# Optimization experiments

Measured on AMD Instinct MI355X. Metric: run time of the kernel, lower is better.

The kernel has to match this reference:

```python
import jax, jax.numpy as jnp
import numpy as np

N_LAYERS = 2
D_MODEL = 768
D_INNER = 1536
D_STATE = 16
D_CONV = 4
DT_RANK = 48
VOCAB = 50257
EPS = 1e-5


def _rms(x, w):
    return x * jax.lax.rsqrt(jnp.mean(x * x, axis=-1, keepdims=True) + EPS) * w


def _mixer(x, in_w, cw, cb, xp_w, dt_w, dt_b, a_log, d_skip, out_w):
    b, l, _ = x.shape
    xz = x @ in_w.T                                  # (b,l,2*d_in)
    u, z = jnp.split(xz, 2, axis=-1)                 # each (b,l,d_in)
    # causal depthwise conv1d
    uc = jax.lax.conv_general_dilated(
        u.transpose(0, 2, 1), cw[:, None, :], (1,), [(D_CONV - 1, 0)],
        feature_group_count=D_INNER, dimension_numbers=("NCH", "OIH", "NCH"))
    u = jax.nn.silu((uc + cb[:, None]).transpose(0, 2, 1))
    x_dbl = u @ xp_w.T                               # (b,l,dt_rank+2n)
    dt, B, C = jnp.split(x_dbl, [DT_RANK, DT_RANK + D_STATE], axis=-1)
    delta = jax.nn.softplus(dt @ dt_w.T + dt_b)      # (b,l,d_in)
    A = -jnp.exp(a_log)                              # (d_in,n)
    dA = jnp.exp(delta[..., None] * A)               # (b,l,d_in,n)
    dBu = delta[..., None] * B[:, :, None, :] * u[..., None]

    def step(h, inp):
        dA_t, dBu_t, C_t = inp
        h = dA_t * h + dBu_t
        return h, jnp.einsum("bdn,bn->bd", h, C_t)

    h0 = jnp.zeros((b, D_INNER, D_STATE), x.dtype)
    _, ys = jax.lax.scan(step, h0, (dA.transpose(1, 0, 2, 3),
                                    dBu.transpose(1, 0, 2, 3),
                                    C.transpose(1, 0, 2)))
    y = ys.transpose(1, 0, 2) + u * d_skip           # (b,l,d_in)
    y = y * jax.nn.silu(z)
    return y @ out_w.T


def setup_inputs() -> dict:
    key = jax.random.key(0)
    ks = jax.random.split(key, 12)
    std = 0.02
    emb = jax.random.normal(ks[0], (VOCAB, D_MODEL), jnp.float32) * std
    emb = emb.at[0].set(0.0)  # padding_idx=0
    tokens = jax.random.randint(ks[1], (2, 1024), 0, VOCAB)
    a_log = jnp.tile(jnp.log(jnp.arange(1, D_STATE + 1, dtype=jnp.float32)),
                     (N_LAYERS, D_INNER, 1))
    return {
        "tokens": tokens,
        "emb": emb,
        "norm_w": jnp.ones((N_LAYERS, D_MODEL), jnp.float32),
        "in_proj_w": jax.random.normal(ks[2], (N_LAYERS, 2 * D_INNER, D_MODEL), jnp.float32) * std,
        "conv_w": jax.random.normal(ks[3], (N_LAYERS, D_INNER, D_CONV), jnp.float32) * 0.1,
        "conv_b": jnp.zeros((N_LAYERS, D_INNER), jnp.float32),
        "x_proj_w": jax.random.normal(ks[4], (N_LAYERS, DT_RANK + 2 * D_STATE, D_INNER), jnp.float32) * std,
        "dt_proj_w": jax.random.normal(ks[5], (N_LAYERS, D_INNER, DT_RANK), jnp.float32) * (DT_RANK ** -0.5),
        "dt_proj_b": jax.random.uniform(ks[6], (N_LAYERS, D_INNER), jnp.float32, -4.6, -2.0),
        "A_log": a_log,
        "D": jnp.ones((N_LAYERS, D_INNER), jnp.float32),
        "out_proj_w": jax.random.normal(ks[7], (N_LAYERS, D_MODEL, D_INNER), jnp.float32) * (std / np.sqrt(2 * N_LAYERS)),
        "normf_w": jnp.ones((D_MODEL,), jnp.float32),
        "lm_head_w": jax.random.normal(ks[8], (VOCAB, D_MODEL), jnp.float32) * std,
    }


def reference(tokens, emb, norm_w, in_proj_w, conv_w, conv_b, x_proj_w,
              dt_proj_w, dt_proj_b, A_log, D, out_proj_w, normf_w, lm_head_w):
    x = emb[tokens]                                  # (b,l,d_model)
    for i in range(N_LAYERS):
        x = x + _mixer(_rms(x, norm_w[i]), in_proj_w[i], conv_w[i], conv_b[i],
                       x_proj_w[i], dt_proj_w[i], dt_proj_b[i], A_log[i],
                       D[i], out_proj_w[i])
    x = _rms(x, normf_w)
    return x @ lm_head_w.T                           # (b,l,vocab)
```

## Files before the change

### kernel.cpp

```cpp
#include <hip/hip_runtime.h>
#include <hip/hip_bf16.h>
#include <math.h>

#define DM 768
#define DI 1536
#define DSN 16
#define NB 2
#define SL 1024
#define MROWS 2048
#define VOC 50257
#define VOCP 50432
#define EPSR 1e-5f

typedef __attribute__((ext_vector_type(8))) short short8;
typedef __attribute__((ext_vector_type(4))) float f32x4;
typedef __attribute__((ext_vector_type(4))) unsigned short us4;
typedef unsigned short u16;

__device__ inline u16 f2bf(float f) {
    unsigned u = __builtin_bit_cast(unsigned, f);
    u += 0x7FFFu + ((u >> 16) & 1u);
    return (u16)(u >> 16);
}

#define G_LDS16(g, l) __builtin_amdgcn_global_load_lds( \
    (const __attribute__((address_space(1))) void*)(g), \
    (__attribute__((address_space(3))) void*)(l), 16, 0, 0)

__global__ __launch_bounds__(256)
void k_embed_rms(const int* __restrict__ tok, const float* __restrict__ emb,
                 const float* __restrict__ w, float* __restrict__ x,
                 u16* __restrict__ out) {
    int r = blockIdx.x;
    int t = tok[r];
    const float* src = emb + (size_t)t * DM;
    int c0 = threadIdx.x * 3;
    float v[3]; float ss = 0.f;
#pragma unroll
    for (int i = 0; i < 3; ++i) {
        v[i] = src[c0 + i]; ss += v[i] * v[i];
        x[(size_t)r * DM + c0 + i] = v[i];
    }
#pragma unroll
    for (int o = 32; o > 0; o >>= 1) ss += __shfl_down(ss, o);
    __shared__ float s[4];
    int lane = threadIdx.x & 63, wv = threadIdx.x >> 6;
    if (lane == 0) s[wv] = ss;
    __syncthreads();
    float sc = rsqrtf((s[0] + s[1] + s[2] + s[3]) / (float)DM + EPSR);
#pragma unroll
    for (int i = 0; i < 3; ++i)
        out[(size_t)r * DM + c0 + i] = f2bf(v[i] * sc * w[c0 + i]);
}

__global__ __launch_bounds__(256)
void k_rmsnorm_bf16(const float* __restrict__ x, const float* __restrict__ w,
                    u16* __restrict__ out) {
    int r = blockIdx.x;
    const float* row = x + (size_t)r * DM;
    int c0 = threadIdx.x * 3;
    float v[3]; float ss = 0.f;
#pragma unroll
    for (int i = 0; i < 3; ++i) { v[i] = row[c0 + i]; ss += v[i] * v[i]; }
#pragma unroll
    for (int o = 32; o > 0; o >>= 1) ss += __shfl_down(ss, o);
    __shared__ float s[4];
    int lane = threadIdx.x & 63, wv = threadIdx.x >> 6;
    if (lane == 0) s[wv] = ss;
    __syncthreads();
    float sc = rsqrtf((s[0] + s[1] + s[2] + s[3]) / (float)DM + EPSR);
#pragma unroll
    for (int i = 0; i < 3; ++i)
        out[(size_t)r * DM + c0 + i] = f2bf(v[i] * sc * w[c0 + i]);
}

struct CvtSeg { const float* src; u16* dst; int sr, sc, sld, dc, blk0, total4; };
struct CvtArgs { CvtSeg seg[9]; };

__global__ __launch_bounds__(256)
void k_cvt_multi(CvtArgs a) {
    int b = blockIdx.x;
    int s = 0;
#pragma unroll
    for (int q = 1; q < 9; ++q) if (a.seg[q].blk0 <= b) s = q;
    const CvtSeg& g = a.seg[s];
    long i4 = (long)(b - g.blk0) * 256 + threadIdx.x;
    if (i4 >= g.total4) return;
    long i = i4 * 4;
    int r = (int)(i / g.dc), c0 = (int)(i % g.dc);
    us4 o;
#pragma unroll
    for (int e = 0; e < 4; ++e) {
        int c = c0 + e;
        float v = (r < g.sr && c < g.sc) ? g.src[(size_t)r * g.sld + c] : 0.f;
        o[e] = f2bf(v);
    }
    *(us4*)&g.dst[i] = o;
}

__global__ void k_cvt_pad4(const float* __restrict__ src, u16* __restrict__ dst,
                           int sr, int sc, int sld, int dc, long total4) {
    long i4 = (long)blockIdx.x * 256 + threadIdx.x;
    if (i4 >= total4) return;
    long i = i4 * 4;
    int r = (int)(i / dc), c0 = (int)(i % dc);
    us4 o;
#pragma unroll
    for (int e = 0; e < 4; ++e) {
        int c = c0 + e;
        float v = (r < sr && c < sc) ? src[(size_t)r * sld + c] : 0.f;
        o[e] = f2bf(v);
    }
    *(us4*)&dst[i] = o;
}

__global__ void k_conv_silu(const float* __restrict__ xz, const float* __restrict__ cw,
                            const float* __restrict__ cb, float* __restrict__ uc,
                            u16* __restrict__ ucb) {
    int d = blockIdx.x * 256 + threadIdx.x;
    int r = blockIdx.y;
    int l = r & (SL - 1);
    float acc = cb[d];
#pragma unroll
    for (int j = 0; j < 4; ++j) {
        int ls = l - 3 + j;
        if (ls >= 0) acc += xz[(size_t)(r - 3 + j) * (2 * DI) + d] * cw[d * 4 + j];
    }
    float s = acc / (1.f + __expf(-acc));
    uc[(size_t)r * DI + d] = s;
    ucb[(size_t)r * DI + d] = f2bf(s);
}

__global__ __launch_bounds__(512)
void k_scan2(const float* __restrict__ delta, const float* __restrict__ uc,
             const float* __restrict__ xdbl, const float* __restrict__ xz,
             const float* __restrict__ alog, const float* __restrict__ Dp,
             u16* __restrict__ ybf) {
    __shared__ float ds2[8][16][20], us2[8][16][20], bn2[8][16][20], cn2[8][16][20];
    __shared__ float Sm[8][16][16], Pm[8][16][16];
    int b  = blockIdx.x / 96;
    int d0 = (blockIdx.x % 96) * 16;
    int tid = threadIdx.x, w = tid >> 6, lane = tid & 63;
    int ch = lane >> 2, nq = lane & 3;
    int d = d0 + ch;
    float A[4];
#pragma unroll
    for (int k = 0; k < 4; ++k) A[k] = -__expf(alog[d * DSN + nq + 4 * k]);
    int tb = w * 128;

    float h[4] = {0.f, 0.f, 0.f, 0.f};
    float sdl = 0.f;
    for (int t0 = 0; t0 < 128; t0 += 16) {
        int row0 = b * SL + tb + t0;
#pragma unroll
        for (int i = 0; i < 4; ++i) {
            int lin = i * 64 + lane, tt = lin >> 4, cc = lin & 15;
            size_t row = (size_t)(row0 + tt);
            ds2[w][cc][tt] = delta[row * DI + d0 + cc];
            us2[w][cc][tt] = uc[row * DI + d0 + cc];
            bn2[w][cc][tt] = xdbl[row * 128 + 48 + cc];
        }
#pragma unroll
        for (int g4 = 0; g4 < 4; ++g4) {
            f32x4 dl = *(const f32x4*)&ds2[w][ch][g4 * 4];
            f32x4 uv = *(const f32x4*)&us2[w][ch][g4 * 4];
            f32x4 bv[4];
#pragma unroll
            for (int k = 0; k < 4; ++k) bv[k] = *(const f32x4*)&bn2[w][nq + 4 * k][g4 * 4];
#pragma unroll
            for (int s = 0; s < 4; ++s) {
                float du = dl[s] * uv[s];
                sdl += dl[s];
#pragma unroll
                for (int k = 0; k < 4; ++k) {
                    float dA = __expf(dl[s] * A[k]);
                    h[k] = h[k] * dA + du * bv[k][s];
                }
            }
        }
    }
#pragma unroll
    for (int k = 0; k < 4; ++k) {
        Sm[w][ch][nq + 4 * k] = h[k];
        Pm[w][ch][nq + 4 * k] = __expf(A[k] * sdl);
    }
    __syncthreads();
    if (tid < 256) {
        int c2 = tid >> 4, n2 = tid & 15;
        float H = 0.f;
#pragma unroll
        for (int g = 0; g < 8; ++g) {
            float hi = H;
            H = Pm[g][c2][n2] * H + Sm[g][c2][n2];
            Sm[g][c2][n2] = hi;
        }
    }
    __syncthreads();
    float Dv = Dp[d];
#pragma unroll
    for (int k = 0; k < 4; ++k) h[k] = Sm[w][ch][nq + 4 * k];
    for (int t0 = 0; t0 < 128; t0 += 16) {
        int row0 = b * SL + tb + t0;
#pragma unroll
        for (int i = 0; i < 4; ++i) {
            int lin = i * 64 + lane, tt = lin >> 4, cc = lin & 15;
            size_t row = (size_t)(row0 + tt);
            ds2[w][cc][tt] = delta[row * DI + d0 + cc];
            us2[w][cc][tt] = uc[row * DI + d0 + cc];
            bn2[w][cc][tt] = xdbl[row * 128 + 48 + cc];
            cn2[w][cc][tt] = xdbl[row * 128 + 64 + cc];
        }
#pragma unroll
        for (int g4 = 0; g4 < 4; ++g4) {
            f32x4 dl = *(const f32x4*)&ds2[w][ch][g4 * 4];
            f32x4 uv = *(const f32x4*)&us2[w][ch][g4 * 4];
            f32x4 bv[4], cv[4];
#pragma unroll
            for (int k = 0; k < 4; ++k) {
                bv[k] = *(const f32x4*)&bn2[w][nq + 4 * k][g4 * 4];
                cv[k] = *(const f32x4*)&cn2[w][nq + 4 * k][g4 * 4];
            }
#pragma unroll
            for (int s = 0; s < 4; ++s) {
                float du = dl[s] * uv[s];
                float p = 0.f;
#pragma unroll
                for (int k = 0; k < 4; ++k) {
                    float dA = __expf(dl[s] * A[k]);
                    h[k] = h[k] * dA + du * bv[k][s];
                    p += h[k] * cv[k][s];
                }
                p += __shfl_xor(p, 1);
                p += __shfl_xor(p, 2);
                if (nq == 0) {
                    size_t row = (size_t)(row0 + g4 * 4 + s);
                    float z = xz[row * (2 * DI) + DI + d];
                    float y = p + uv[s] * Dv;
                    y *= z / (1.f + __expf(-z));
                    ybf[row * DI + d] = f2bf(y);
                }
            }
        }
    }
}

template <int EPIL>
__global__ __launch_bounds__(256)
void k_gemm_bt(const u16* __restrict__ A, const u16* __restrict__ W,
               float* C, const float* RES,
               const float* __restrict__ BIASV,
               int K, int ldc, int nTm) {
    __shared__ u16 Al[128 * 32];
    __shared__ u16 Wl[128 * 32];
    int nwg = gridDim.x;
    int qc = nwg >> 3, rc = nwg & 7;
    int xcd = blockIdx.x & 7, j = blockIdx.x >> 3;
    int wg = (xcd < rc ? xcd * (qc + 1) : rc * (qc + 1) + (xcd - rc) * qc) + j;
    int m0 = (wg % nTm) * 128, n0 = (wg / nTm) * 128;

    int tid = threadIdx.x, wave = tid >> 6, lane = tid & 63;
    int wm = wave >> 1, wn = wave & 1;
    f32x4 acc[4][4] = {};
    const int rS = (lane >> 2);
    const int kS = (((lane & 3) ^ ((lane >> 3) & 3)) * 8);
    const int kofs = (((lane >> 4) ^ ((lane >> 1) & 3)) * 8);
    const int fr = lane & 15;

    for (int k0 = 0; k0 < K; k0 += 32) {
#pragma unroll
        for (int i = 0; i < 2; ++i) {
            int rowA = m0 + wave * 32 + i * 16 + rS;
            G_LDS16(A + (size_t)rowA * K + k0 + kS, &Al[wave * 1024 + i * 512]);
            int rowW = n0 + wave * 32 + i * 16 + rS;
            G_LDS16(W + (size_t)rowW * K + k0 + kS, &Wl[wave * 1024 + i * 512]);
        }
        __syncthreads();
        short8 af[4], bfr[4];
#pragma unroll
        for (int f = 0; f < 4; ++f) {
            af[f]  = *(const short8*)&Al[(wm * 64 + f * 16 + fr) * 32 + kofs];
            bfr[f] = *(const short8*)&Wl[(wn * 64 + f * 16 + fr) * 32 + kofs];
        }
#pragma unroll
        for (int i = 0; i < 4; ++i)
#pragma unroll
            for (int jj = 0; jj < 4; ++jj)
                acc[i][jj] = __builtin_amdgcn_mfma_f32_16x16x32_bf16(af[i], bfr[jj], acc[i][jj], 0, 0, 0);
        __syncthreads();
    }
    int r4 = (lane >> 4) * 4;
#pragma unroll
    for (int i = 0; i < 4; ++i)
#pragma unroll
        for (int jj = 0; jj < 4; ++jj) {
            int col = n0 + wn * 64 + jj * 16 + fr;
            float bia = (EPIL == 2) ? BIASV[col] : 0.f;
#pragma unroll
            for (int rr = 0; rr < 4; ++rr) {
                int row = m0 + wm * 64 + i * 16 + r4 + rr;
                size_t off = (size_t)row * ldc + col;
                float v = acc[i][jj][rr];
                if (EPIL == 1) v += RES[off];
                if (EPIL == 2) { v += bia; v = (v > 20.f) ? v : log1pf(__expf(v)); }
                C[off] = v;
            }
        }
}

#define BAR  __builtin_amdgcn_s_barrier()
#define LGK0 do { asm volatile("s_waitcnt lgkmcnt(0)" ::: "memory"); \
                  __builtin_amdgcn_sched_barrier(0); } while (0)
#define VMC6 asm volatile("s_waitcnt vmcnt(6)" ::: "memory")
#define VMC0 asm volatile("s_waitcnt vmcnt(0)" ::: "memory")

#define STAGE_HT(t, op, half, GB, RB) do {                                   \
    const u16* _g = (GB) + (size_t)((RB) + (half) * 128 + (w << 3) + srow) * K \
                    + (t) * 64 + scol;                                        \
    G_LDS16(_g, &lds[(t) & 1][op][half][w << 9]);                             \
    G_LDS16(_g + (size_t)64 * K, &lds[(t) & 1][op][half][4096 + (w << 9)]);   \
} while (0)

#define RD_A(dst, t, mq) do {                                                \
    _Pragma("unroll") for (int _m = 0; _m < 4; ++_m)                          \
    _Pragma("unroll") for (int _k = 0; _k < 2; ++_k)                          \
        dst[_m][_k] = *(const short8*)&lds[(t) & 1][0][wm]                    \
            [(mq) * 4096 + _m * 1024 + (rd_off ^ (_k << 5))];                 \
} while (0)

#define RD_B(t, nq) do {                                                     \
    _Pragma("unroll") for (int _n = 0; _n < 2; ++_n)                          \
    _Pragma("unroll") for (int _k = 0; _k < 2; ++_k)                          \
        bfv[_n][_k] = *(const short8*)&lds[(t) & 1][1][wbh]                   \
            [wbr * 4096 + (nq) * 2048 + _n * 1024 + (rd_off ^ (_k << 5))];    \
} while (0)

#define MM16(AF, mq, nq) do {                                                \
    __builtin_amdgcn_s_setprio(1);                                           \
    _Pragma("unroll") for (int _m = 0; _m < 4; ++_m)                          \
    _Pragma("unroll") for (int _n = 0; _n < 2; ++_n)                          \
    _Pragma("unroll") for (int _k = 0; _k < 2; ++_k)                          \
        acc[(mq) * 4 + _m][(nq) * 2 + _n] =                                   \
            __builtin_amdgcn_mfma_f32_16x16x32_bf16(                          \
                AF[_m][_k], bfv[_n][_k], acc[(mq) * 4 + _m][(nq) * 2 + _n],   \
                0, 0, 0);                                                     \
    __builtin_amdgcn_s_setprio(0);                                           \
} while (0)

template <int K>
__global__ __launch_bounds__(512, 2)
void k_gemm256(const u16* __restrict__ Ap, const u16* __restrict__ Wp,
               float* __restrict__ C, int ldc, int nmax, int nTm) {
    constexpr int NT = K / 64;
    constexpr int NI = NT / 2;
    __shared__ __align__(16) u16 lds[2][2][2][8192];

    int per8 = gridDim.x >> 3;
    int wg = (blockIdx.x & 7) * per8 + (blockIdx.x >> 3);
    int m0 = (wg % nTm) * 256, n0 = (wg / nTm) * 256;

    int tid = threadIdx.x, w = tid >> 6, lane = tid & 63;
    int wm = w >> 2, wn = w & 3, wbh = wn >> 1, wbr = wn & 1;
    int fr = lane & 15;
    int sw = (fr & 1) * 32 + ((fr >> 1) & 1) * 16 + ((fr >> 2) & 1) * 8;
    int rd_off = fr * 64 + (((lane >> 4) * 8) ^ sw);
    int srow = lane >> 3;
    int scol = ((lane & 7) * 8) ^ (((lane >> 3) & 1) * 32 + ((lane >> 4) & 1) * 16 +
                                   ((lane >> 5) & 1) * 8);

    f32x4 acc[8][4] = {};
    short8 af0[4][2], af1[4][2], bfv[2][2];

    STAGE_HT(0, 0, 0, Ap, m0); STAGE_HT(0, 0, 1, Ap, m0);
    STAGE_HT(0, 1, 0, Wp, n0); STAGE_HT(0, 1, 1, Wp, n0);
    STAGE_HT(1, 0, 0, Ap, m0); STAGE_HT(1, 0, 1, Ap, m0);
    STAGE_HT(1, 1, 0, Wp, n0);
    VMC6; BAR;

    for (int i = 0; i < NI - 1; ++i) {
        const int ta = 2 * i, tb = 2 * i + 1;
        RD_A(af0, ta, 0); RD_B(ta, 0);
        STAGE_HT(tb, 1, 1, Wp, n0);
        BAR; LGK0; MM16(af0, 0, 0); BAR;
        RD_A(af1, ta, 1);
        STAGE_HT(ta + 2, 0, 0, Ap, m0);
        BAR; LGK0; MM16(af1, 1, 0); BAR;
        RD_B(ta, 1);
        STAGE_HT(ta + 2, 0, 1, Ap, m0);
        BAR; LGK0; MM16(af1, 1, 1); BAR;
        STAGE_HT(ta + 2, 1, 0, Wp, n0);
        BAR; MM16(af0, 0, 1); VMC6; BAR;
        RD_A(af0, tb, 0); RD_B(tb, 0);
        STAGE_HT(ta + 2, 1, 1, Wp, n0);
        BAR; LGK0; MM16(af0, 0, 0); BAR;
        RD_A(af1, tb, 1);
        STAGE_HT(ta + 3, 0, 0, Ap, m0);
        BAR; LGK0; MM16(af1, 1, 0); BAR;
        RD_B(tb, 1);
        STAGE_HT(ta + 3, 0, 1, Ap, m0);
        BAR; LGK0; MM16(af1, 1, 1); BAR;
        STAGE_HT(ta + 3, 1, 0, Wp, n0);
        BAR; MM16(af0, 0, 1); VMC6; BAR;
    }
    {
        const int ta = NT - 2, tb = NT - 1;
        RD_A(af0, ta, 0); RD_B(ta, 0);
        STAGE_HT(tb, 1, 1, Wp, n0);
        BAR; LGK0; MM16(af0, 0, 0); BAR;
        RD_A(af1, ta, 1);
        BAR; LGK0; MM16(af1, 1, 0); BAR;
        RD_B(ta, 1);
        BAR; LGK0; MM16(af1, 1, 1); BAR;
        BAR; MM16(af0, 0, 1); VMC0; BAR;
        RD_A(af0, tb, 0); RD_B(tb, 0);
        BAR; LGK0; MM16(af0, 0, 0); BAR;
        RD_A(af1, tb, 1);
        BAR; LGK0; MM16(af1, 1, 0); BAR;
        RD_B(tb, 1);
        BAR; LGK0; MM16(af1, 1, 1); BAR;
        BAR; MM16(af0, 0, 1); BAR;
    }

    int r4 = (lane >> 4) * 4;
#pragma unroll
    for (int mi = 0; mi < 8; ++mi)
#pragma unroll
        for (int ni = 0; ni < 4; ++ni) {
            int col = n0 + wn * 64 + (ni >> 1) * 32 + (ni & 1) * 16 + fr;
            if (col >= nmax) continue;
            int row = m0 + wm * 128 + (mi >> 2) * 64 + (mi & 3) * 16 + r4;
#pragma unroll
            for (int rr = 0; rr < 4; ++rr)
                C[(size_t)(row + rr) * ldc + col] = acc[mi][ni][rr];
        }
}

extern "C" void kernel_launch(void* const* d_in, const int* in_sizes, int n_in,
                              void* d_out, int out_size, void* d_ws, size_t ws_size,
                              hipStream_t stream) {
    (void)in_sizes; (void)n_in; (void)out_size;
    const int*   tok   = (const int*)d_in[0];
    const float* emb   = (const float*)d_in[1];
    const float* normw = (const float*)d_in[2];
    const float* inw   = (const float*)d_in[3];
    const float* cw    = (const float*)d_in[4];
    const float* cb    = (const float*)d_in[5];
    const float* xpw   = (const float*)d_in[6];
    const float* dtw   = (const float*)d_in[7];
    const float* dtb   = (const float*)d_in[8];
    const float* alog  = (const float*)d_in[9];
    const float* Dp    = (const float*)d_in[10];
    const float* outw  = (const float*)d_in[11];
    const float* normf = (const float*)d_in[12];
    const float* lmw   = (const float*)d_in[13];
    float* out = (float*)d_out;

    char* p = (char*)d_ws;
    auto alloc = [&](size_t bytes) { char* r = p; p += (bytes + 255) & ~(size_t)255; return r; };
    float* x     = (float*)alloc((size_t)MROWS * DM * 4);
    u16*   xnb   = (u16*)  alloc((size_t)MROWS * DM * 2);
    float* xz    = (float*)alloc((size_t)MROWS * 2 * DI * 4);
    float* uc    = (float*)alloc((size_t)MROWS * DI * 4);
    u16*   ucb   = (u16*)  alloc((size_t)MROWS * DI * 2);
    float* xdbl  = (float*)alloc((size_t)MROWS * 128 * 4);
    u16*   xdblb = (u16*)  alloc((size_t)MROWS * 64 * 2);
    float* delta = (float*)alloc((size_t)MROWS * DI * 4);
    u16*   ybf   = (u16*)  alloc((size_t)MROWS * DI * 2);
    u16*   winb  = (u16*)  alloc((size_t)NB * (2 * DI) * DM * 2);
    u16*   wxpb  = (u16*)  alloc((size_t)NB * 128 * DI * 2);
    u16*   wdtb  = (u16*)  alloc((size_t)NB * DI * 64 * 2);
    u16*   woutb = (u16*)  alloc((size_t)NB * DM * DI * 2);
    u16*   wlmb  = (u16*)  alloc((size_t)VOCP * DM * 2);
    if ((size_t)(p - (char*)d_ws) > ws_size) return;

    CvtArgs ca;
    int blk = 0;
    auto seg = [&](int idx, const float* s, u16* d, int sr, int sc, int sld, int dc, int dr) {
        int t4 = dr * dc / 4;
        ca.seg[idx] = CvtSeg{s, d, sr, sc, sld, dc, blk, t4};
        blk += (t4 + 255) / 256;
    };
    seg(0, lmw, wlmb, VOC, DM, DM, DM, VOCP);
    seg(1, inw,                          winb,                          2 * DI, DM, DM, DM, 2 * DI);
    seg(2, inw + (size_t)2 * DI * DM,    winb + (size_t)2 * DI * DM,    2 * DI, DM, DM, DM, 2 * DI);
    seg(3, xpw,                          wxpb,                          80, DI, DI, DI, 128);
    seg(4, xpw + (size_t)80 * DI,        wxpb + (size_t)128 * DI,       80, DI, DI, DI, 128);
    seg(5, dtw,                          wdtb,                          DI, 48, 48, 64, DI);
    seg(6, dtw + (size_t)DI * 48,        wdtb + (size_t)DI * 64,        DI, 48, 48, 64, DI);
    seg(7, outw,                         woutb,                         DM, DI, DI, DI, DM);
    seg(8, outw + (size_t)DM * DI,       woutb + (size_t)DM * DI,       DM, DI, DI, DI, DM);
    k_cvt_multi<<<dim3(blk), 256, 0, stream>>>(ca);

    k_embed_rms<<<MROWS, 256, 0, stream>>>(tok, emb, normw, x, xnb);

    for (int i = 0; i < NB; ++i) {
        if (i > 0)
            k_rmsnorm_bf16<<<MROWS, 256, 0, stream>>>(x, normw + i * DM, xnb);

        k_gemm_bt<0><<<dim3(16 * (2 * DI / 128)), 256, 0, stream>>>(
            xnb, winb + (size_t)i * 2 * DI * DM, xz, nullptr, nullptr, DM, 2 * DI, 16);

        k_conv_silu<<<dim3(DI / 256, MROWS), 256, 0, stream>>>(
            xz, cw + (size_t)i * DI * 4, cb + (size_t)i * DI, uc, ucb);

        k_gemm_bt<0><<<dim3(16 * 1), 256, 0, stream>>>(
            ucb, wxpb + (size_t)i * 128 * DI, xdbl, nullptr, nullptr, DI, 128, 16);

        { long t4 = (long)MROWS * 64 / 4;
          k_cvt_pad4<<<dim3((unsigned)((t4 + 255) / 256)), 256, 0, stream>>>(
              xdbl, xdblb, MROWS, 64, 128, 64, t4); }

        k_gemm_bt<2><<<dim3(16 * (DI / 128)), 256, 0, stream>>>(
            xdblb, wdtb + (size_t)i * DI * 64, delta, nullptr, dtb + (size_t)i * DI,
            64, DI, 16);

        k_scan2<<<dim3(NB * (DI / 16)), 512, 0, stream>>>(
            delta, uc, xdbl, xz, alog + (size_t)i * DI * DSN, Dp + i * DI, ybf);

        k_gemm_bt<1><<<dim3(16 * (DM / 128)), 256, 0, stream>>>(
            ybf, woutb + (size_t)i * DM * DI, x, x, nullptr, DI, DM, 16);
    }

    k_rmsnorm_bf16<<<MROWS, 256, 0, stream>>>(x, normf, xnb);
    k_gemm256<DM><<<dim3(8 * (VOCP / 256)), 512, 0, stream>>>(
        xnb, wlmb, out, VOC, VOC, 8);
}
```

Before: 793.6 us.

## Halve GEMM K-tile to 32 and raise occupancy target to four blocks

Reworks the 256x256 GEMM pipeline to use a K-step of 32 instead of 64. This halves the LDS footprint per block (64KB to 32KB), cuts fragment registers, and requests launch bounds of 4 blocks per CU. Staging, swizzle patterns and vmcnt waits are rewritten to match the smaller tile. In exchange there are twice as many barrier-heavy pipeline stages per K, so synchronisation overhead per MFMA doubles, and register pressure under the higher occupancy bound may force spills.

Result: slower. 2.487 ms (+213.3%).

```diff
diff --git a/kernel.cpp b/kernel.cpp
--- a/kernel.cpp
+++ b/kernel.cpp
@@ -310,49 +310,44 @@
 #define BAR  __builtin_amdgcn_s_barrier()
 #define LGK0 do { asm volatile("s_waitcnt lgkmcnt(0)" ::: "memory"); \
                   __builtin_amdgcn_sched_barrier(0); } while (0)
-#define VMC6 asm volatile("s_waitcnt vmcnt(6)" ::: "memory")
+#define VMC3 asm volatile("s_waitcnt vmcnt(3)" ::: "memory")
 #define VMC0 asm volatile("s_waitcnt vmcnt(0)" ::: "memory")
 
-#define STAGE_HT(t, op, half, GB, RB) do {                                   \
-    const u16* _g = (GB) + (size_t)((RB) + (half) * 128 + (w << 3) + srow) * K \
-                    + (t) * 64 + scol;                                        \
-    G_LDS16(_g, &lds[(t) & 1][op][half][w << 9]);                             \
-    G_LDS16(_g + (size_t)64 * K, &lds[(t) & 1][op][half][4096 + (w << 9)]);   \
+#define STAGE1(t, op, half, GB, RB) do {                                      \
+    const u16* _g = (GB) + (size_t)((RB) + (half) * 128 + (w << 4) + srow) * K \
+                    + (t) * 32 + scol;                                         \
+    G_LDS16(_g, &lds[(t) & 1][op][half][w << 9]);                              \
 } while (0)
 
-#define RD_A(dst, t, mq) do {                                                \
-    _Pragma("unroll") for (int _m = 0; _m < 4; ++_m)                          \
-    _Pragma("unroll") for (int _k = 0; _k < 2; ++_k)                          \
-        dst[_m][_k] = *(const short8*)&lds[(t) & 1][0][wm]                    \
-            [(mq) * 4096 + _m * 1024 + (rd_off ^ (_k << 5))];                 \
+#define RDA(dst, t, mq) do {                                                   \
+    _Pragma("unroll") for (int _m = 0; _m < 4; ++_m)                           \
+        dst[_m] = *(const short8*)&lds[(t) & 1][0][wm]                         \
+            [((mq) * 64 + _m * 16 + fr) * 32 + rd_sw];                         \
 } while (0)
 
-#define RD_B(t, nq) do {                                                     \
-    _Pragma("unroll") for (int _n = 0; _n < 2; ++_n)                          \
-    _Pragma("unroll") for (int _k = 0; _k < 2; ++_k)                          \
-        bfv[_n][_k] = *(const short8*)&lds[(t) & 1][1][wbh]                   \
-            [wbr * 4096 + (nq) * 2048 + _n * 1024 + (rd_off ^ (_k << 5))];    \
+#define RDB(t, nq) do {                                                       \
+    _Pragma("unroll") for (int _n = 0; _n < 2; ++_n)                           \
+        bfv[_n] = *(const short8*)&lds[(t) & 1][1][wbh]                        \
+            [(wbr * 64 + (nq) * 32 + _n * 16 + fr) * 32 + rd_sw];              \
 } while (0)
 
-#define MM16(AF, mq, nq) do {                                                \
-    __builtin_amdgcn_s_setprio(1);                                           \
-    _Pragma("unroll") for (int _m = 0; _m < 4; ++_m)                          \
-    _Pragma("unroll") for (int _n = 0; _n < 2; ++_n)                          \
-    _Pragma("unroll") for (int _k = 0; _k < 2; ++_k)                          \
-        acc[(mq) * 4 + _m][(nq) * 2 + _n] =                                   \
-            __builtin_amdgcn_mfma_f32_16x16x32_bf16(                          \
-                AF[_m][_k], bfv[_n][_k], acc[(mq) * 4 + _m][(nq) * 2 + _n],   \
-                0, 0, 0);                                                     \
-    __builtin_amdgcn_s_setprio(0);                                           \
+#define MM8(AF, mq, nq) do {                                                  \
+    __builtin_amdgcn_s_setprio(1);                                            \
+    _Pragma("unroll") for (int _m = 0; _m < 4; ++_m)                           \
+    _Pragma("unroll") for (int _n = 0; _n < 2; ++_n)                           \
+        acc[(mq) * 4 + _m][(nq) * 2 + _n] =                                    \
+            __builtin_amdgcn_mfma_f32_16x16x32_bf16(                           \
+                AF[_m], bfv[_n], acc[(mq) * 4 + _m][(nq) * 2 + _n], 0, 0, 0);  \
+    __builtin_amdgcn_s_setprio(0);                                            \
 } while (0)
 
 template <int K>
-__global__ __launch_bounds__(512, 2)
+__global__ __launch_bounds__(512, 4)
 void k_gemm256(const u16* __restrict__ Ap, const u16* __restrict__ Wp,
                float* __restrict__ C, int ldc, int nmax, int nTm) {
-    constexpr int NT = K / 64;
+    constexpr int NT = K / 32;
     constexpr int NI = NT / 2;
-    __shared__ __align__(16) u16 lds[2][2][2][8192];
+    __shared__ __align__(16) u16 lds[2][2][2][4096];
 
     int per8 = gridDim.x >> 3;
     int wg = (blockIdx.x & 7) * per8 + (blockIdx.x >> 3);
@@ -361,63 +356,61 @@
     int tid = threadIdx.x, w = tid >> 6, lane = tid & 63;
     int wm = w >> 2, wn = w & 3, wbh = wn >> 1, wbr = wn & 1;
     int fr = lane & 15;
-    int sw = (fr & 1) * 32 + ((fr >> 1) & 1) * 16 + ((fr >> 2) & 1) * 8;
-    int rd_off = fr * 64 + (((lane >> 4) * 8) ^ sw);
-    int srow = lane >> 3;
-    int scol = ((lane & 7) * 8) ^ (((lane >> 3) & 1) * 32 + ((lane >> 4) & 1) * 16 +
-                                   ((lane >> 5) & 1) * 8);
+    int rd_sw = (((lane >> 4) ^ ((lane >> 1) & 3)) * 8);
+    int srow  = lane >> 2;
+    int scol  = (((lane & 3) ^ ((lane >> 3) & 3)) * 8);
 
     f32x4 acc[8][4] = {};
-    short8 af0[4][2], af1[4][2], bfv[2][2];
-
-    STAGE_HT(0, 0, 0, Ap, m0); STAGE_HT(0, 0, 1, Ap, m0);
-    STAGE_HT(0, 1, 0, Wp, n0); STAGE_HT(0, 1, 1, Wp, n0);
-    STAGE_HT(1, 0, 0, Ap, m0); STAGE_HT(1, 0, 1, Ap, m0);
-    STAGE_HT(1, 1, 0, Wp, n0);
-    VMC6; BAR;
+    short8 af0[4], af1[4], bfv[2];
+
+    STAGE1(0, 0, 0, Ap, m0); STAGE1(0, 0, 1, Ap, m0);
+    STAGE1(0, 1, 0, Wp, n0); STAGE1(0, 1, 1, Wp, n0);
+    STAGE1(1, 0, 0, Ap, m0); STAGE1(1, 0, 1, Ap, m0);
+    STAGE1(1, 1, 0, Wp, n0);
+    VMC3; BAR;
 
     for (int i = 0; i < NI - 1; ++i) {
         const int ta = 2 * i, tb = 2 * i + 1;
-        RD_A(af0, ta, 0); RD_B(ta, 0);
-        STAGE_HT(tb, 1, 1, Wp, n0);
-        BAR; LGK0; MM16(af0, 0, 0); BAR;
-        RD_A(af1, ta, 1);
-        STAGE_HT(ta + 2, 0, 0, Ap, m0);
-        BAR; LGK0; MM16(af1, 1, 0); BAR;
-        RD_B(ta, 1);
-        STAGE_HT(ta + 2, 0, 1, Ap, m0);
-        BAR; LGK0; MM16(af1, 1, 1); BAR;
-        STAGE_HT(ta + 2, 1, 0, Wp, n0);
-        BAR; MM16(af0, 0, 1); VMC6; BAR;
-        RD_A(af0, tb, 0); RD_B(tb, 0);
-        STAGE_HT(ta + 2, 1, 1, Wp, n0);
-        BAR; LGK0; MM16(af0, 0, 0); BAR;
-        RD_A(af1, tb, 1);
-        STAGE_HT(ta + 3, 0, 0, Ap, m0);
-        BAR; LGK0; MM16(af1, 1, 0); BAR;
-        RD_B(tb, 1);
-        STAGE_HT(ta + 3, 0, 1, Ap, m0);
-        BAR; LGK0; MM16(af1, 1, 1); BAR;
-        STAGE_HT(ta + 3, 1, 0, Wp, n0);
-        BAR; MM16(af0, 0, 1); VMC6; BAR;
+        RDA(af0, ta, 0); RDB(ta, 0);
+        STAGE1(tb, 1, 1, Wp, n0);
+        BAR; LGK0; MM8(af0, 0, 0); BAR;
+        RDA(af1, ta, 1);
+        STAGE1(ta + 2, 0, 0, Ap, m0);
+        BAR; LGK0; MM8(af1, 1, 0); BAR;
+        RDB(ta, 1);
+        STAGE1(ta + 2, 0, 1, Ap, m0);
+        BAR; LGK0; MM8(af1, 1, 1); BAR;
+        STAGE1(ta + 2, 1, 0, Wp, n0);
+        BAR; MM8(af0, 0, 1); VMC3; BAR;
+        RDA(af0, tb, 0); RDB(tb, 0);
+        STAGE1(ta + 2, 1, 1, Wp, n0);
+        BAR; LGK0; MM8(af0, 0, 0); BAR;
+        RDA(af1, tb, 1);
+        STAGE1(ta + 3, 0, 0, Ap, m0);
+        BAR; LGK0; MM8(af1, 1, 0); BAR;
+        RDB(tb, 1);
+        STAGE1(ta + 3, 0, 1, Ap, m0);
+        BAR; LGK0; MM8(af1, 1, 1); BAR;
+        STAGE1(ta + 3, 1, 0, Wp, n0);
+        BAR; MM8(af0, 0, 1); VMC3; BAR;
     }
     {
         const int ta = NT - 2, tb = NT - 1;
-        RD_A(af0, ta, 0); RD_B(ta, 0);
-        STAGE_HT(tb, 1, 1, Wp, n0);
-        BAR; LGK0; MM16(af0, 0, 0); BAR;
-        RD_A(af1, ta, 1);
-        BAR; LGK0; MM16(af1, 1, 0); BAR;
-        RD_B(ta, 1);
-        BAR; LGK0; MM16(af1, 1, 1); BAR;
-        BAR; MM16(af0, 0, 1); VMC0; BAR;
-        RD_A(af0, tb, 0); RD_B(tb, 0);
-        BAR; LGK0; MM16(af0, 0, 0); BAR;
-        RD_A(af1, tb, 1);
-        BAR; LGK0; MM16(af1, 1, 0); BAR;
-        RD_B(tb, 1);
-        BAR; LGK0; MM16(af1, 1, 1); BAR;
-        BAR; MM16(af0, 0, 1); BAR;
+        RDA(af0, ta, 0); RDB(ta, 0);
+        STAGE1(tb, 1, 1, Wp, n0);
+        BAR; LGK0; MM8(af0, 0, 0); BAR;
+        RDA(af1, ta, 1);
+        BAR; LGK0; MM8(af1, 1, 0); BAR;
+        RDB(ta, 1);
+        BAR; LGK0; MM8(af1, 1, 1); BAR;
+        BAR; MM8(af0, 0, 1); VMC0; BAR;
+        RDA(af0, tb, 0); RDB(tb, 0);
+        BAR; LGK0; MM8(af0, 0, 0); BAR;
+        RDA(af1, tb, 1);
+        BAR; LGK0; MM8(af1, 1, 0); BAR;
+        RDB(tb, 1);
+        BAR; LGK0; MM8(af1, 1, 1); BAR;
+        BAR; MM8(af0, 0, 1); BAR;
     }
 
     int r4 = (lane >> 4) * 4;
```
